# Performance work log

Measured on AMD Instinct MI355X. Metric: run time of the kernel, lower is better.

Reference implementation:

```python
import jax, jax.numpy as jnp
import numpy as np

B, C, L, H = 4, 16, 512, 1024

def setup_inputs() -> dict:
    key = jax.random.key(0)
    k1, k2, k3 = jax.random.split(key, 3)
    start_hidden = jax.random.normal(k1, (B, C, L, H), dtype=jnp.float32)
    end_hidden = jax.random.normal(k2, (B, C, L, H), dtype=jnp.float32)
    # learned scoring vector v of size start_size + end_size = 2H, uniform(-0.1, 0.1)
    v = jax.random.uniform(k3, (2 * H,), dtype=jnp.float32, minval=-0.1, maxval=0.1)
    return {"start_hidden": start_hidden, "end_hidden": end_hidden, "v": v}

def reference(start_hidden, end_hidden, v):
    # Original math: res[b,c,i,j] = concat(start[b,c,i], end[b,c,j]) . v
    # which decomposes exactly as start[b,c,i].v[:H] + end[b,c,j].v[H:]
    h = start_hidden.shape[-1]
    s = jnp.einsum('bclh,h->bcl', start_hidden, v[:h])   # [B,C,L]
    e = jnp.einsum('bclh,h->bcl', end_hidden, v[h:])     # [B,C,L]
    res = s[:, :, :, None] + e[:, :, None, :]            # [B,C,L,L]
    return jnp.transpose(res, (0, 2, 3, 1))              # [B,L,L,C]
```

## Files before the change

### kernel.cpp

```cpp
#include <hip/hip_runtime.h>

#define B_ 4
#define C_ 16
#define L_ 512
#define H_ 1024

__global__ __launch_bounds__(256) void dot_kernel(const float4* __restrict__ start,
                                                  const float4* __restrict__ endp,
                                                  const float4* __restrict__ v,
                                                  float* __restrict__ se) {
    const int lane       = threadIdx.x & 63;
    const int waveInBlk  = threadIdx.x >> 6;
    const int gwave      = blockIdx.x * (blockDim.x >> 6) + waveInBlk;
    const int nwaves     = gridDim.x * (blockDim.x >> 6);
    const int rows_half  = B_ * C_ * L_;
    const int total_rows = 2 * rows_half;

    float4 vs[4], ve[4];
#pragma unroll
    for (int k = 0; k < 4; ++k) {
        vs[k] = v[k * 64 + lane];
        ve[k] = v[H_ / 4 + k * 64 + lane];
    }

    for (int row = gwave; row < total_rows; row += nwaves) {
        const int half = row >> 15;
        const int r    = row & (rows_half - 1);
        const float4* in = (half ? endp : start) + (size_t)r * (H_ / 4);

        float acc = 0.f;
#pragma unroll
        for (int k = 0; k < 4; ++k) {
            float4 x  = in[k * 64 + lane];
            float4 vv = half ? ve[k] : vs[k];
            acc += x.x * vv.x + x.y * vv.y + x.z * vv.z + x.w * vv.w;
        }
#pragma unroll
        for (int m = 32; m > 0; m >>= 1) acc += __shfl_xor(acc, m, 64);

        if (lane == 0) {
            const int b = r / (C_ * L_);
            const int c = (r / L_) & (C_ - 1);
            const int l = r & (L_ - 1);
            se[half * (B_ * L_ * C_) + (b * L_ + l) * C_ + c] = acc;
        }
    }
}

__global__ __launch_bounds__(256) void outer_kernel(const float4* __restrict__ se4,
                                                    float4* __restrict__ out4) {
    const int t  = blockIdx.x * blockDim.x + threadIdx.x;
    const int cq = t & 3;
    const int j  = (t >> 2) & (L_ - 1);
    const int bi = t >> 11;
    float4 s = se4[bi * 4 + cq];
    const int b = bi >> 9;
    float4 e = se4[(B_ * L_ * 4) + (b * L_ + j) * 4 + cq];
    out4[t] = make_float4(s.x + e.x, s.y + e.y, s.z + e.z, s.w + e.w);
}

extern "C" void kernel_launch(void* const* d_in, const int* in_sizes, int n_in,
                              void* d_out, int out_size, void* d_ws, size_t ws_size,
                              hipStream_t stream) {
    const float4* start = (const float4*)d_in[0];
    const float4* endp  = (const float4*)d_in[1];
    const float4* v     = (const float4*)d_in[2];
    float*        se    = (float*)d_ws;
    float4*       out4  = (float4*)d_out;

    dot_kernel<<<2048, 256, 0, stream>>>(start, endp, v, se);

    outer_kernel<<<16384, 256, 0, stream>>>((const float4*)se, out4);
}
```

Measured before the change: 297.8 us.

## Batch four rows per wave in dot kernel and widen outer-kernel per-block work

The dot kernel now gives each wave four fixed rows instead of a grid-stride loop. It issues all 16 float4 loads up front to raise memory-level parallelism, then does four interleaved shuffle reductions and launches 4096 blocks. The outer kernel uses one block per (b,i) row and loads the s vector once, with each thread writing eight float4 outputs. This cuts index math and redundant loads. The cost is higher register pressure, and the grid mapping is hardcoded to these exact sizes.

```diff
diff --git a/kernel.cpp b/kernel.cpp
--- a/kernel.cpp
+++ b/kernel.cpp
@@ -9,54 +9,75 @@
                                                   const float4* __restrict__ endp,
                                                   const float4* __restrict__ v,
                                                   float* __restrict__ se) {
-    const int lane       = threadIdx.x & 63;
-    const int waveInBlk  = threadIdx.x >> 6;
-    const int gwave      = blockIdx.x * (blockDim.x >> 6) + waveInBlk;
-    const int nwaves     = gridDim.x * (blockDim.x >> 6);
-    const int rows_half  = B_ * C_ * L_;
-    const int total_rows = 2 * rows_half;
+    const int lane = threadIdx.x & 63;
+    const int wv   = (blockIdx.x << 2) | (threadIdx.x >> 6);
+    const int half = wv >> 13;
+    const int r0   = (wv & 8191) << 2;
 
-    float4 vs[4], ve[4];
+    const float4* __restrict__ base = half ? endp : start;
+    const float4* __restrict__ vh   = v + half * (H_ / 4);
+
+    float4 vf[4];
 #pragma unroll
-    for (int k = 0; k < 4; ++k) {
-        vs[k] = v[k * 64 + lane];
-        ve[k] = v[H_ / 4 + k * 64 + lane];
+    for (int k = 0; k < 4; ++k) vf[k] = vh[k * 64 + lane];
+
+    float4 x[4][4];
+#pragma unroll
+    for (int r = 0; r < 4; ++r) {
+        const float4* in = base + (size_t)(r0 + r) * (H_ / 4);
+#pragma unroll
+        for (int k = 0; k < 4; ++k) x[r][k] = in[k * 64 + lane];
     }
 
-    for (int row = gwave; row < total_rows; row += nwaves) {
-        const int half = row >> 15;
-        const int r    = row & (rows_half - 1);
-        const float4* in = (half ? endp : start) + (size_t)r * (H_ / 4);
+    float acc[4];
+#pragma unroll
+    for (int r = 0; r < 4; ++r) {
+        float a = 0.f;
+#pragma unroll
+        for (int k = 0; k < 4; ++k)
+            a += x[r][k].x * vf[k].x + x[r][k].y * vf[k].y +
+                 x[r][k].z * vf[k].z + x[r][k].w * vf[k].w;
+        acc[r] = a;
+    }
 
-        float acc = 0.f;
 #pragma unroll
-        for (int k = 0; k < 4; ++k) {
-            float4 x  = in[k * 64 + lane];
-            float4 vv = half ? ve[k] : vs[k];
-            acc += x.x * vv.x + x.y * vv.y + x.z * vv.z + x.w * vv.w;
-        }
+    for (int m = 32; m > 0; m >>= 1) {
 #pragma unroll
-        for (int m = 32; m > 0; m >>= 1) acc += __shfl_xor(acc, m, 64);
+        for (int r = 0; r < 4; ++r) acc[r] += __shfl_xor(acc[r], m, 64);
+    }
 
-        if (lane == 0) {
-            const int b = r / (C_ * L_);
-            const int c = (r / L_) & (C_ - 1);
-            const int l = r & (L_ - 1);
-            se[half * (B_ * L_ * C_) + (b * L_ + l) * C_ + c] = acc;
-        }
+    if (lane == 0) {
+        const int b  = r0 >> 13;
+        const int c  = (r0 >> 9) & (C_ - 1);
+        const int l0 = r0 & (L_ - 1);
+        float* p = se + (half << 15) + (((b << 9) | l0) << 4) + c;
+#pragma unroll
+        for (int r = 0; r < 4; ++r) p[r << 4] = acc[r];
     }
 }
 
 __global__ __launch_bounds__(256) void outer_kernel(const float4* __restrict__ se4,
                                                     float4* __restrict__ out4) {
-    const int t  = blockIdx.x * blockDim.x + threadIdx.x;
-    const int cq = t & 3;
-    const int j  = (t >> 2) & (L_ - 1);
-    const int bi = t >> 11;
-    float4 s = se4[bi * 4 + cq];
-    const int b = bi >> 9;
-    float4 e = se4[(B_ * L_ * 4) + (b * L_ + j) * 4 + cq];
-    out4[t] = make_float4(s.x + e.x, s.y + e.y, s.z + e.z, s.w + e.w);
+    const int bi  = blockIdx.x;
+    const int b   = bi >> 9;
+    const int tid = threadIdx.x;
+
+    const float4 s = se4[(bi << 2) | (tid & 3)];
+    const float4* __restrict__ e = se4 + (B_ * L_ * 4) + (b << 11);
+    float4* __restrict__ o = out4 + (size_t)bi * (L_ * C_ / 4);
+
+    float4 ev[8];
+#pragma unroll
+    for (int it = 0; it < 8; ++it) ev[it] = e[it * 256 + tid];
+#pragma unroll
+    for (int it = 0; it < 8; ++it) {
+        float4 r;
+        r.x = s.x + ev[it].x;
+        r.y = s.y + ev[it].y;
+        r.z = s.z + ev[it].z;
+        r.w = s.w + ev[it].w;
+        o[it * 256 + tid] = r;
+    }
 }
 
 extern "C" void kernel_launch(void* const* d_in, const int* in_sizes, int n_in,
@@ -68,7 +89,7 @@
     float*        se    = (float*)d_ws;
     float4*       out4  = (float4*)d_out;
 
-    dot_kernel<<<2048, 256, 0, stream>>>(start, endp, v, se);
+    dot_kernel<<<4096, 256, 0, stream>>>(start, endp, v, se);
 
-    outer_kernel<<<16384, 256, 0, stream>>>((const float4*)se, out4);
+    outer_kernel<<<B_ * L_, 256, 0, stream>>>((const float4*)se, out4);
 }
```

Result: no change. 299.3 us (+0.5%).
